# Kernel optimization log

Measured on AMD Instinct MI355X. Metric: run time of the kernel, lower is better.

Reference implementation:

```python
import jax, jax.numpy as jnp
import numpy as np

N_GROUPS = 1024   # n
L = 128           # keys per group
R = 4             # queries per group (nq[i] == R)
NQ_TOTAL = N_GROUPS * R
D_Q = 256
D_K = 256
D_Z = 256
D_V = 256


def setup_inputs() -> dict:
    key = jax.random.key(0)
    ks = jax.random.split(key, 8)
    nq = jnp.full((N_GROUPS,), R, dtype=jnp.int32)
    q = jax.random.normal(ks[0], (NQ_TOTAL, D_Q), dtype=jnp.float32)
    k = jax.random.normal(ks[1], (N_GROUPS, L, D_K), dtype=jnp.float32)
    v = jax.random.normal(ks[2], (N_GROUPS, L, D_V), dtype=jnp.float32)
    m = jax.random.uniform(ks[3], (N_GROUPS, L)) < 0.9
    m = m.at[:, 0].set(True)  # guarantee each row has at least one valid key
    Wq = jax.random.normal(ks[4], (D_Q, D_Z), dtype=jnp.float32) / np.sqrt(D_Q)
    bq = jnp.zeros((D_Z,), dtype=jnp.float32)
    Wk = jax.random.normal(ks[5], (D_K, D_Z), dtype=jnp.float32) / np.sqrt(D_K)
    bk = jnp.zeros((D_Z,), dtype=jnp.float32)
    return {"nq": nq, "q": q, "k": k, "v": v, "m": m,
            "Wq": Wq, "bq": bq, "Wk": Wk, "bk": bk}


def reference(nq, q, v, k, m, Wq, bq, Wk, bk):
    # Linear projections (nn.Linear with bias)
    qz = q @ Wq + bq                      # (N, d_z)
    kz = k @ Wk + bk                      # (n, l, d_z)
    d_z = Wq.shape[1]
    n = m.shape[0]
    # group index per query: equivalent to repeat_interleave(nq, 0)
    gidx = jnp.repeat(jnp.arange(n), nq, total_repeat_length=q.shape[0])  # (N,)
    # scores: s[i, l] = <kz[group(i), l], qz[i]> / sqrt(d_z)
    s = jnp.einsum('ild,id->il', kz[gidx], qz) / jnp.sqrt(jnp.asarray(d_z, qz.dtype))
    s = jnp.where(m[gidx], s, -jnp.inf)   # masked_fill(~m, -inf)
    p = jax.nn.softmax(s, axis=-1)        # softmax over key dim l
    # weighted sum over keys: (N, d)
    return jnp.einsum('il,ild->id', p, v[gidx])
```

## Files before the change

### kernel.cpp

```cpp
#include <hip/hip_runtime.h>

#define D 256
#define LKEYS 128
#define NGROUP 1024
#define NQ 4096

#define MMAT_OFF 0
#define RVEC_OFF (D * D)
#define U_OFF    (RVEC_OFF + D)
#define WS_FLOATS (U_OFF + NQ * D)

#define DOT4(a, b) ((a).x*(b).x + (a).y*(b).y + (a).z*(b).z + (a).w*(b).w)

__device__ __forceinline__ void gload_lds16(const float* g, float* l) {
    __builtin_amdgcn_global_load_lds(
        (const __attribute__((address_space(1))) void*)g,
        (__attribute__((address_space(3))) void*)l, 16, 0, 0);
}

__global__ __launch_bounds__(256) void prep_kernel(
    const float* __restrict__ Wq, const float* __restrict__ Wk,
    const float* __restrict__ bq, float* __restrict__ Mmat,
    float* __restrict__ rvec)
{
    __shared__ float wq_s[32][65];
    __shared__ float wk_s[32][65];
    __shared__ float bq_s[64];
    const int t  = threadIdx.x;
    const int a0 = (int)(blockIdx.x >> 3) * 32;
    const int b0 = (int)(blockIdx.x & 7) * 32;
    const int ai = t >> 4;
    const int bj = t & 15;
    float acc00 = 0.f, acc01 = 0.f, acc10 = 0.f, acc11 = 0.f;
    float racc = 0.f;
    for (int z0 = 0; z0 < D; z0 += 64) {
        __syncthreads();
        #pragma unroll
        for (int i = 0; i < 2; ++i) {
            const int f4i = t + 256 * i;
            const int row = f4i >> 4;
            const int c   = (f4i & 15) * 4;
            float4 aa = *(const float4*)&Wq[(size_t)(a0 + row) * D + z0 + c];
            wq_s[row][c] = aa.x; wq_s[row][c+1] = aa.y; wq_s[row][c+2] = aa.z; wq_s[row][c+3] = aa.w;
            float4 bb = *(const float4*)&Wk[(size_t)(b0 + row) * D + z0 + c];
            wk_s[row][c] = bb.x; wk_s[row][c+1] = bb.y; wk_s[row][c+2] = bb.z; wk_s[row][c+3] = bb.w;
        }
        if (t < 64) bq_s[t] = bq[z0 + t];
        __syncthreads();
        #pragma unroll 8
        for (int z = 0; z < 64; ++z) {
            const float wq0 = wq_s[ai][z];
            const float wq1 = wq_s[ai + 16][z];
            const float wk0 = wk_s[bj][z];
            const float wk1 = wk_s[bj + 16][z];
            acc00 += wq0 * wk0; acc01 += wq0 * wk1;
            acc10 += wq1 * wk0; acc11 += wq1 * wk1;
        }
        if (a0 == 0 && t < 32) {
            #pragma unroll 8
            for (int z = 0; z < 64; ++z) racc += bq_s[z] * wk_s[t][z];
        }
    }
    Mmat[(size_t)(a0 + ai)      * D + b0 + bj]      = acc00;
    Mmat[(size_t)(a0 + ai)      * D + b0 + bj + 16] = acc01;
    Mmat[(size_t)(a0 + ai + 16) * D + b0 + bj]      = acc10;
    Mmat[(size_t)(a0 + ai + 16) * D + b0 + bj + 16] = acc11;
    if (a0 == 0 && t < 32) rvec[b0 + t] = racc;
}

__global__ __launch_bounds__(256) void u_gemm_kernel(
    const float* __restrict__ q, const float* __restrict__ Mmat,
    const float* __restrict__ rvec, float* __restrict__ uout)
{
    __shared__ float q_s[16][D];
    const int b = blockIdx.x, t = threadIdx.x, lane = t & 63, w = t >> 6;
    {
        const float4* qg = (const float4*)(q + (size_t)b * 16 * D);
        float4* qs4 = (float4*)q_s;
        #pragma unroll
        for (int i = 0; i < 4; ++i) qs4[t + 256 * i] = qg[t + 256 * i];
    }
    __syncthreads();

    const float4* M4 = (const float4*)Mmat;
    const int r0 = w * 4;
    float4 a0 = {0,0,0,0}, a1 = {0,0,0,0}, a2 = {0,0,0,0}, a3 = {0,0,0,0};
    #pragma unroll 4
    for (int kk = 0; kk < D; ++kk) {
        const float4 m4 = M4[kk * 64 + lane];
        const float qa = q_s[r0 + 0][kk], qb = q_s[r0 + 1][kk];
        const float qc = q_s[r0 + 2][kk], qd = q_s[r0 + 3][kk];
        a0.x += qa*m4.x; a0.y += qa*m4.y; a0.z += qa*m4.z; a0.w += qa*m4.w;
        a1.x += qb*m4.x; a1.y += qb*m4.y; a1.z += qb*m4.z; a1.w += qb*m4.w;
        a2.x += qc*m4.x; a2.y += qc*m4.y; a2.z += qc*m4.z; a2.w += qc*m4.w;
        a3.x += qd*m4.x; a3.y += qd*m4.y; a3.z += qd*m4.z; a3.w += qd*m4.w;
    }
    const float4 r4 = ((const float4*)rvec)[lane];
    float4* U4 = (float4*)uout;
    float4 o;
    o.x=(a0.x+r4.x)*0.0625f; o.y=(a0.y+r4.y)*0.0625f; o.z=(a0.z+r4.z)*0.0625f; o.w=(a0.w+r4.w)*0.0625f;
    U4[((size_t)b * 16 + r0 + 0) * 64 + lane] = o;
    o.x=(a1.x+r4.x)*0.0625f; o.y=(a1.y+r4.y)*0.0625f; o.z=(a1.z+r4.z)*0.0625f; o.w=(a1.w+r4.w)*0.0625f;
    U4[((size_t)b * 16 + r0 + 1) * 64 + lane] = o;
    o.x=(a2.x+r4.x)*0.0625f; o.y=(a2.y+r4.y)*0.0625f; o.z=(a2.z+r4.z)*0.0625f; o.w=(a2.w+r4.w)*0.0625f;
    U4[((size_t)b * 16 + r0 + 2) * 64 + lane] = o;
    o.x=(a3.x+r4.x)*0.0625f; o.y=(a3.y+r4.y)*0.0625f; o.z=(a3.z+r4.z)*0.0625f; o.w=(a3.w+r4.w)*0.0625f;
    U4[((size_t)b * 16 + r0 + 3) * 64 + lane] = o;
}

__global__ __launch_bounds__(256) void attn2_kernel(
    const float* __restrict__ k, const float* __restrict__ v,
    const int* __restrict__ m, const float* __restrict__ uws,
    float* __restrict__ out)
{
    const int g = blockIdx.x, t = threadIdx.x, lane = t & 63, w = t >> 6;

    __shared__ float buf[2][16 * D];
    __shared__ float p_s[4][LKEYS];
    __shared__ int   m_s[LKEYS];

    const float* kg = k + (size_t)g * LKEYS * D;
    const float* vg = v + (size_t)g * LKEYS * D;

    auto stage = [&](const float* src, int tile, int b) {
        const float* s = src + (size_t)tile * 16 * D;
        #pragma unroll
        for (int j = 0; j < 4; ++j) {
            const int r = w * 4 + j;
            gload_lds16(s + r * D + lane * 4, &buf[b][r * D]);
        }
    };

    stage(kg, 0, 0);
    if (t < LKEYS) m_s[t] = m[(size_t)g * LKEYS + t];

    const float4* U4 = (const float4*)uws;
    const float4 u0 = U4[((size_t)g * 4 + 0) * 64 + lane];
    const float4 u1 = U4[((size_t)g * 4 + 1) * 64 + lane];
    const float4 u2 = U4[((size_t)g * 4 + 2) * 64 + lane];
    const float4 u3 = U4[((size_t)g * 4 + 3) * 64 + lane];
    __syncthreads();

    for (int tl = 0; tl < 8; ++tl) {
        if (tl < 7) stage(kg, tl + 1, (tl + 1) & 1);

        const float4* B4 = (const float4*)&buf[tl & 1][0];
        const int kb = w * 4;
        const float4 ka0 = B4[(kb + 0) * 64 + lane];
        const float4 ka1 = B4[(kb + 1) * 64 + lane];
        const float4 ka2 = B4[(kb + 2) * 64 + lane];
        const float4 ka3 = B4[(kb + 3) * 64 + lane];

        float v16[16];
        v16[ 0]=DOT4(ka0,u0); v16[ 1]=DOT4(ka0,u1); v16[ 2]=DOT4(ka0,u2); v16[ 3]=DOT4(ka0,u3);
        v16[ 4]=DOT4(ka1,u0); v16[ 5]=DOT4(ka1,u1); v16[ 6]=DOT4(ka1,u2); v16[ 7]=DOT4(ka1,u3);
        v16[ 8]=DOT4(ka2,u0); v16[ 9]=DOT4(ka2,u1); v16[10]=DOT4(ka2,u2); v16[11]=DOT4(ka2,u3);
        v16[12]=DOT4(ka3,u0); v16[13]=DOT4(ka3,u1); v16[14]=DOT4(ka3,u2); v16[15]=DOT4(ka3,u3);

        float v8[8];
        { const int hb = lane & 1;
          #pragma unroll
          for (int i = 0; i < 8; ++i) {
              const float keep = hb ? v16[8 + i] : v16[i];
              const float send = hb ? v16[i]     : v16[8 + i];
              v8[i] = keep + __shfl_xor(send, 1);
          } }
        float v4a[4];
        { const int hb = (lane >> 1) & 1;
          #pragma unroll
          for (int i = 0; i < 4; ++i) {
              const float keep = hb ? v8[4 + i] : v8[i];
              const float send = hb ? v8[i]     : v8[4 + i];
              v4a[i] = keep + __shfl_xor(send, 2);
          } }
        float v2a[2];
        { const int hb = (lane >> 2) & 1;
          #pragma unroll
          for (int i = 0; i < 2; ++i) {
              const float keep = hb ? v4a[2 + i] : v4a[i];
              const float send = hb ? v4a[i]     : v4a[2 + i];
              v2a[i] = keep + __shfl_xor(send, 4);
          } }
        float v1;
        { const int hb = (lane >> 3) & 1;
          const float keep = hb ? v2a[1] : v2a[0];
          const float send = hb ? v2a[0] : v2a[1];
          v1 = keep + __shfl_xor(send, 8); }
        v1 += __shfl_xor(v1, 16);
        v1 += __shfl_xor(v1, 32);

        if (lane < 16) {
            const int i  = ((lane & 1) << 3) | ((lane & 2) << 1) | ((lane & 4) >> 1) | ((lane & 8) >> 3);
            const int kl = tl * 16 + w * 4 + (i >> 2);
            p_s[i & 3][kl] = m_s[kl] ? v1 : -1e30f;
        }
        __syncthreads();
    }

    stage(vg, 0, 0);
    {
        const float s0 = p_s[w][lane];
        const float s1 = p_s[w][lane + 64];
        float mx = fmaxf(s0, s1);
        #pragma unroll
        for (int off = 32; off > 0; off >>= 1) mx = fmaxf(mx, __shfl_xor(mx, off));
        const float e0 = __expf(s0 - mx);
        const float e1 = __expf(s1 - mx);
        float sm = e0 + e1;
        #pragma unroll
        for (int off = 32; off > 0; off >>= 1) sm += __shfl_xor(sm, off);
        const float inv = 1.0f / sm;
        p_s[w][lane]      = e0 * inv;
        p_s[w][lane + 64] = e1 * inv;
    }
    __syncthreads();

    float4 acc = {0, 0, 0, 0};
    for (int tl = 0; tl < 8; ++tl) {
        if (tl < 7) stage(vg, tl + 1, (tl + 1) & 1);
        const float4* B4 = (const float4*)&buf[tl & 1][0];
        #pragma unroll
        for (int r = 0; r < 16; ++r) {
            const float pw = p_s[w][tl * 16 + r];
            const float4 vv = B4[r * 64 + lane];
            acc.x += pw * vv.x; acc.y += pw * vv.y;
            acc.z += pw * vv.z; acc.w += pw * vv.w;
        }
        __syncthreads();
    }
    ((float4*)(out + ((size_t)g * 4 + w) * D))[lane] = acc;
}

__global__ __launch_bounds__(256) void attn_kernel(
    const float* __restrict__ q, const float* __restrict__ k,
    const float* __restrict__ v, const int* __restrict__ m,
    const float* __restrict__ Mmat, const float* __restrict__ rvec,
    float* __restrict__ out)
{
    const int g    = blockIdx.x;
    const int t    = threadIdx.x;
    const int lane = t & 63;
    const int w    = t >> 6;

    __shared__ float  q_s[4][D];
    __shared__ float4 part_s[4][4][64];
    __shared__ float4 u_s4[4][64];
    __shared__ float  p_s[4][LKEYS];
    __shared__ int    m_s[LKEYS];

    {
        const float4* qg = (const float4*)(q + (size_t)g * 4 * D);
        ((float4*)q_s)[t] = qg[t];
    }
    if (t < LKEYS) m_s[t] = m[(size_t)g * LKEYS + t];
    __syncthreads();
    {
        const float4* M4 = (const float4*)Mmat;
        float4 p0 = {0,0,0,0}, p1 = {0,0,0,0}, p2 = {0,0,0,0}, p3 = {0,0,0,0};
        const int base = w * 64;
        #pragma unroll 4
        for (int dd = 0; dd < 64; ++dd) {
            const int a = base + dd;
            const float4 m4 = M4[a * 64 + lane];
            const float q0 = q_s[0][a], q1 = q_s[1][a], q2 = q_s[2][a], q3 = q_s[3][a];
            p0.x += q0*m4.x; p0.y += q0*m4.y; p0.z += q0*m4.z; p0.w += q0*m4.w;
            p1.x += q1*m4.x; p1.y += q1*m4.y; p1.z += q1*m4.z; p1.w += q1*m4.w;
            p2.x += q2*m4.x; p2.y += q2*m4.y; p2.z += q2*m4.z; p2.w += q2*m4.w;
            p3.x += q3*m4.x; p3.y += q3*m4.y; p3.z += q3*m4.z; p3.w += q3*m4.w;
        }
        part_s[w][0][lane] = p0; part_s[w][1][lane] = p1;
        part_s[w][2][lane] = p2; part_s[w][3][lane] = p3;
    }
    __syncthreads();
    {
        float4 acc = ((const float4*)rvec)[lane];
        const float4 a0 = part_s[0][w][lane], a1 = part_s[1][w][lane];
        const float4 a2 = part_s[2][w][lane], a3 = part_s[3][w][lane];
        acc.x += a0.x + a1.x + a2.x + a3.x;
        acc.y += a0.y + a1.y + a2.y + a3.y;
        acc.z += a0.z + a1.z + a2.z + a3.z;
        acc.w += a0.w + a1.w + a2.w + a3.w;
        u_s4[w][lane] = acc;
    }
    __syncthreads();

    const float4 u0 = u_s4[0][lane], u1 = u_s4[1][lane];
    const float4 u2 = u_s4[2][lane], u3 = u_s4[3][lane];
    {
        const float4* kg = (const float4*)(k + (size_t)g * LKEYS * D);
        auto reduce_qt = [&](float d0, float d1, float d2, float d3) -> float {
            float keepA = (lane & 1) ? d1 : d0;
            float sendA = (lane & 1) ? d0 : d1;
            keepA += __shfl_xor(sendA, 1);
            float keepB = (lane & 1) ? d3 : d2;
            float sendB = (lane & 1) ? d2 : d3;
            keepB += __shfl_xor(sendB, 1);
            float keep = (lane & 2) ? keepB : keepA;
            float send = (lane & 2) ? keepA : keepB;
            keep += __shfl_xor(send, 2);
            keep += __shfl_xor(keep, 4);
            keep += __shfl_xor(keep, 8);
            keep += __shfl_xor(keep, 16);
            keep += __shfl_xor(keep, 32);
            return keep;
        };
        const int l0 = w * 32;
        for (int kk = 0; kk < 32; kk += 4) {
            const int l = l0 + kk;
            const float4 kA = kg[(l + 0) * 64 + lane];
            const float4 kB = kg[(l + 1) * 64 + lane];
            const float4 kC = kg[(l + 2) * 64 + lane];
            const float4 kD = kg[(l + 3) * 64 + lane];
            float dA0 = DOT4(kA,u0), dA1 = DOT4(kA,u1), dA2 = DOT4(kA,u2), dA3 = DOT4(kA,u3);
            float dB0 = DOT4(kB,u0), dB1 = DOT4(kB,u1), dB2 = DOT4(kB,u2), dB3 = DOT4(kB,u3);
            float dC0 = DOT4(kC,u0), dC1 = DOT4(kC,u1), dC2 = DOT4(kC,u2), dC3 = DOT4(kC,u3);
            float dD0 = DOT4(kD,u0), dD1 = DOT4(kD,u1), dD2 = DOT4(kD,u2), dD3 = DOT4(kD,u3);
            const float rA = reduce_qt(dA0, dA1, dA2, dA3);
            const float rB = reduce_qt(dB0, dB1, dB2, dB3);
            const float rC = reduce_qt(dC0, dC1, dC2, dC3);
            const float rD = reduce_qt(dD0, dD1, dD2, dD3);
            if (lane < 4) {
                p_s[lane][l + 0] = m_s[l + 0] ? rA * 0.0625f : -1e30f;
                p_s[lane][l + 1] = m_s[l + 1] ? rB * 0.0625f : -1e30f;
                p_s[lane][l + 2] = m_s[l + 2] ? rC * 0.0625f : -1e30f;
                p_s[lane][l + 3] = m_s[l + 3] ? rD * 0.0625f : -1e30f;
            }
        }
    }
    __syncthreads();
    {
        const float v0 = p_s[w][lane];
        const float v1 = p_s[w][lane + 64];
        float mx = fmaxf(v0, v1);
        #pragma unroll
        for (int off = 32; off > 0; off >>= 1) mx = fmaxf(mx, __shfl_xor(mx, off));
        const float e0 = __expf(v0 - mx);
        const float e1 = __expf(v1 - mx);
        float sm = e0 + e1;
        #pragma unroll
        for (int off = 32; off > 0; off >>= 1) sm += __shfl_xor(sm, off);
        const float inv = 1.0f / sm;
        p_s[w][lane]      = e0 * inv;
        p_s[w][lane + 64] = e1 * inv;
    }
    {
        const float4* vg = (const float4*)(v + (size_t)g * LKEYS * D);
        float4 acc = {0,0,0,0};
        #pragma unroll 8
        for (int l = 0; l < LKEYS; ++l) {
            const float pw = p_s[w][l];
            const float4 vv = vg[l * 64 + lane];
            acc.x += pw * vv.x; acc.y += pw * vv.y;
            acc.z += pw * vv.z; acc.w += pw * vv.w;
        }
        float4* og = (float4*)(out + ((size_t)g * 4 + w) * D);
        og[lane] = acc;
    }
}

extern "C" void kernel_launch(void* const* d_in, const int* in_sizes, int n_in,
                              void* d_out, int out_size, void* d_ws, size_t ws_size,
                              hipStream_t stream) {
    const float* q  = (const float*)d_in[1];
    const float* k  = (const float*)d_in[2];
    const float* v  = (const float*)d_in[3];
    const int*   m  = (const int*)  d_in[4];
    const float* Wq = (const float*)d_in[5];
    const float* bq = (const float*)d_in[6];
    const float* Wk = (const float*)d_in[7];

    float* ws = (float*)d_ws;
    prep_kernel<<<64, 256, 0, stream>>>(Wq, Wk, bq, ws + MMAT_OFF, ws + RVEC_OFF);

    if (ws_size >= (size_t)WS_FLOATS * sizeof(float)) {
        u_gemm_kernel<<<NQ / 16, 256, 0, stream>>>(q, ws + MMAT_OFF, ws + RVEC_OFF, ws + U_OFF);
        attn2_kernel<<<NGROUP, 256, 0, stream>>>(k, v, m, ws + U_OFF, (float*)d_out);
    } else {
        attn_kernel<<<NGROUP, 256, 0, stream>>>(q, k, v, m, ws + MMAT_OFF, ws + RVEC_OFF,
                                                (float*)d_out);
    }
}
```

Before: 81.14 us.

## Give each wave a private key slice and ring buffer to drop block barriers

The attention kernel is restructured so each wave owns 32 keys and a private 8-row LDS ring, streaming K then V through it with explicit vmcnt waits instead of block-wide __syncthreads per tile. The mask becomes a wave ballot, the softmax normalisation is deferred to the end, and partial P·V sums from the four waves are reduced through LDS. This is meant to remove per-tile barrier stalls and overlap V prefetch with the score phase. The cost is an extra cross-wave reduction and reliance on hand-placed waitcnt ordering, which is fragile.

```diff
diff --git a/kernel.cpp b/kernel.cpp
--- a/kernel.cpp
+++ b/kernel.cpp
@@ -17,6 +17,11 @@
         (const __attribute__((address_space(1))) void*)g,
         (__attribute__((address_space(3))) void*)l, 16, 0, 0);
 }
+
+#define WAITVM(N) do { asm volatile("s_waitcnt vmcnt(" #N ")" ::: "memory"); \
+                       __builtin_amdgcn_sched_barrier(0); } while (0)
+#define WAITLG0   do { asm volatile("s_waitcnt lgkmcnt(0)" ::: "memory"); \
+                       __builtin_amdgcn_sched_barrier(0); } while (0)
 
 __global__ __launch_bounds__(256) void prep_kernel(
     const float* __restrict__ Wq, const float* __restrict__ Wk,
@@ -108,54 +113,65 @@
     U4[((size_t)b * 16 + r0 + 3) * 64 + lane] = o;
 }
 
-__global__ __launch_bounds__(256) void attn2_kernel(
+__global__ __launch_bounds__(256, 4) void attn3_kernel(
     const float* __restrict__ k, const float* __restrict__ v,
     const int* __restrict__ m, const float* __restrict__ uws,
     float* __restrict__ out)
 {
     const int g = blockIdx.x, t = threadIdx.x, lane = t & 63, w = t >> 6;
 
-    __shared__ float buf[2][16 * D];
-    __shared__ float p_s[4][LKEYS];
-    __shared__ int   m_s[LKEYS];
-
-    const float* kg = k + (size_t)g * LKEYS * D;
-    const float* vg = v + (size_t)g * LKEYS * D;
-
-    auto stage = [&](const float* src, int tile, int b) {
-        const float* s = src + (size_t)tile * 16 * D;
-        #pragma unroll
-        for (int j = 0; j < 4; ++j) {
-            const int r = w * 4 + j;
-            gload_lds16(s + r * D + lane * 4, &buf[b][r * D]);
-        }
+    __shared__ float smem[4 * 8 * D + LKEYS * 4];
+    float* const myring = smem + w * 8 * D;
+    float* const p_t    = smem + 4 * 8 * D;
+
+    const int mk = (lane < 32) ? m[(size_t)g * LKEYS + w * 32 + lane] : 0;
+    const unsigned long long bal = __ballot(mk != 0);
+
+    const float4* U4 = (const float4*)(uws + (size_t)g * 4 * D);
+    const float4 u0 = U4[0 * 64 + lane];
+    const float4 u1 = U4[1 * 64 + lane];
+    const float4 u2 = U4[2 * 64 + lane];
+    const float4 u3 = U4[3 * 64 + lane];
+    asm volatile("s_waitcnt vmcnt(0)" ::: "memory");
+    __builtin_amdgcn_sched_barrier(0);
+
+    const float* kg = k + ((size_t)g * LKEYS + w * 32) * D;
+    const float* vg = v + ((size_t)g * LKEYS + w * 32) * D;
+
+    auto issueK = [&](int c) {
+        const int sl = (4 * c) & 7;
+        #pragma unroll
+        for (int j = 0; j < 4; ++j)
+            gload_lds16(kg + (size_t)(4 * c + j) * D + lane * 4, myring + (sl + j) * D);
     };
-
-    stage(kg, 0, 0);
-    if (t < LKEYS) m_s[t] = m[(size_t)g * LKEYS + t];
-
-    const float4* U4 = (const float4*)uws;
-    const float4 u0 = U4[((size_t)g * 4 + 0) * 64 + lane];
-    const float4 u1 = U4[((size_t)g * 4 + 1) * 64 + lane];
-    const float4 u2 = U4[((size_t)g * 4 + 2) * 64 + lane];
-    const float4 u3 = U4[((size_t)g * 4 + 3) * 64 + lane];
-    __syncthreads();
-
-    for (int tl = 0; tl < 8; ++tl) {
-        if (tl < 7) stage(kg, tl + 1, (tl + 1) & 1);
-
-        const float4* B4 = (const float4*)&buf[tl & 1][0];
-        const int kb = w * 4;
-        const float4 ka0 = B4[(kb + 0) * 64 + lane];
-        const float4 ka1 = B4[(kb + 1) * 64 + lane];
-        const float4 ka2 = B4[(kb + 2) * 64 + lane];
-        const float4 ka3 = B4[(kb + 3) * 64 + lane];
+    auto issueV = [&](int c) {
+        const int sl = (4 * c) & 7;
+        #pragma unroll
+        for (int j = 0; j < 4; ++j)
+            gload_lds16(vg + (size_t)(4 * c + j) * D + lane * 4, myring + (sl + j) * D);
+    };
+
+    issueK(0); issueK(1);
+
+    #pragma unroll
+    for (int c = 0; c < 8; ++c) {
+        WAITVM(4);
+        const int sl = (4 * c) & 7;
+        const float4* R = (const float4*)myring;
+        const float4 k0 = R[(sl + 0) * 64 + lane];
+        const float4 k1 = R[(sl + 1) * 64 + lane];
+        const float4 k2 = R[(sl + 2) * 64 + lane];
+        const float4 k3 = R[(sl + 3) * 64 + lane];
+        WAITLG0;
+        if (c < 6)       issueK(c + 2);
+        else if (c == 6) issueV(0);
+        else             issueV(1);
 
         float v16[16];
-        v16[ 0]=DOT4(ka0,u0); v16[ 1]=DOT4(ka0,u1); v16[ 2]=DOT4(ka0,u2); v16[ 3]=DOT4(ka0,u3);
-        v16[ 4]=DOT4(ka1,u0); v16[ 5]=DOT4(ka1,u1); v16[ 6]=DOT4(ka1,u2); v16[ 7]=DOT4(ka1,u3);
-        v16[ 8]=DOT4(ka2,u0); v16[ 9]=DOT4(ka2,u1); v16[10]=DOT4(ka2,u2); v16[11]=DOT4(ka2,u3);
-        v16[12]=DOT4(ka3,u0); v16[13]=DOT4(ka3,u1); v16[14]=DOT4(ka3,u2); v16[15]=DOT4(ka3,u3);
+        v16[ 0]=DOT4(k0,u0); v16[ 1]=DOT4(k0,u1); v16[ 2]=DOT4(k0,u2); v16[ 3]=DOT4(k0,u3);
+        v16[ 4]=DOT4(k1,u0); v16[ 5]=DOT4(k1,u1); v16[ 6]=DOT4(k1,u2); v16[ 7]=DOT4(k1,u3);
+        v16[ 8]=DOT4(k2,u0); v16[ 9]=DOT4(k2,u1); v16[10]=DOT4(k2,u2); v16[11]=DOT4(k2,u3);
+        v16[12]=DOT4(k3,u0); v16[13]=DOT4(k3,u1); v16[14]=DOT4(k3,u2); v16[15]=DOT4(k3,u3);
 
         float v8[8];
         { const int hb = lane & 1;
@@ -191,44 +207,89 @@
 
         if (lane < 16) {
             const int i  = ((lane & 1) << 3) | ((lane & 2) << 1) | ((lane & 4) >> 1) | ((lane & 8) >> 3);
-            const int kl = tl * 16 + w * 4 + (i >> 2);
-            p_s[i & 3][kl] = m_s[kl] ? v1 : -1e30f;
-        }
-        __syncthreads();
-    }
-
-    stage(vg, 0, 0);
-    {
-        const float s0 = p_s[w][lane];
-        const float s1 = p_s[w][lane + 64];
+            const int kl = 4 * c + (i >> 2);
+            p_t[(w * 32 + kl) * 4 + (i & 3)] = ((bal >> kl) & 1ull) ? v1 : -1e30f;
+        }
+    }
+
+    WAITLG0;
+    __builtin_amdgcn_s_barrier();
+
+    float inv;
+    {
+        const float s0 = p_t[lane * 4 + w];
+        const float s1 = p_t[(lane + 64) * 4 + w];
         float mx = fmaxf(s0, s1);
         #pragma unroll
         for (int off = 32; off > 0; off >>= 1) mx = fmaxf(mx, __shfl_xor(mx, off));
         const float e0 = __expf(s0 - mx);
         const float e1 = __expf(s1 - mx);
-        float sm = e0 + e1;
-        #pragma unroll
-        for (int off = 32; off > 0; off >>= 1) sm += __shfl_xor(sm, off);
-        const float inv = 1.0f / sm;
-        p_s[w][lane]      = e0 * inv;
-        p_s[w][lane + 64] = e1 * inv;
-    }
-    __syncthreads();
-
-    float4 acc = {0, 0, 0, 0};
-    for (int tl = 0; tl < 8; ++tl) {
-        if (tl < 7) stage(vg, tl + 1, (tl + 1) & 1);
-        const float4* B4 = (const float4*)&buf[tl & 1][0];
-        #pragma unroll
-        for (int r = 0; r < 16; ++r) {
-            const float pw = p_s[w][tl * 16 + r];
-            const float4 vv = B4[r * 64 + lane];
-            acc.x += pw * vv.x; acc.y += pw * vv.y;
-            acc.z += pw * vv.z; acc.w += pw * vv.w;
-        }
-        __syncthreads();
-    }
-    ((float4*)(out + ((size_t)g * 4 + w) * D))[lane] = acc;
+        float su = e0 + e1;
+        #pragma unroll
+        for (int off = 32; off > 0; off >>= 1) su += __shfl_xor(su, off);
+        inv = 1.0f / su;
+        p_t[lane * 4 + w]        = e0;
+        p_t[(lane + 64) * 4 + w] = e1;
+    }
+    WAITLG0;
+    __builtin_amdgcn_s_barrier();
+
+    float4 a0 = {0,0,0,0}, a1 = {0,0,0,0}, a2 = {0,0,0,0}, a3 = {0,0,0,0};
+    #pragma unroll
+    for (int c = 0; c < 8; ++c) {
+        if (c < 7) { WAITVM(4); } else { WAITVM(0); }
+        const int sl = (4 * c) & 7;
+        const float4* R = (const float4*)myring;
+        const float4 w0 = R[(sl + 0) * 64 + lane];
+        const float4 w1 = R[(sl + 1) * 64 + lane];
+        const float4 w2 = R[(sl + 2) * 64 + lane];
+        const float4 w3 = R[(sl + 3) * 64 + lane];
+        const float4 p0 = *(const float4*)&p_t[(w * 32 + 4 * c + 0) * 4];
+        const float4 p1 = *(const float4*)&p_t[(w * 32 + 4 * c + 1) * 4];
+        const float4 p2 = *(const float4*)&p_t[(w * 32 + 4 * c + 2) * 4];
+        const float4 p3 = *(const float4*)&p_t[(w * 32 + 4 * c + 3) * 4];
+        WAITLG0;
+        if (c < 6) issueV(c + 2);
+
+        a0.x += p0.x*w0.x; a0.y += p0.x*w0.y; a0.z += p0.x*w0.z; a0.w += p0.x*w0.w;
+        a1.x += p0.y*w0.x; a1.y += p0.y*w0.y; a1.z += p0.y*w0.z; a1.w += p0.y*w0.w;
+        a2.x += p0.z*w0.x; a2.y += p0.z*w0.y; a2.z += p0.z*w0.z; a2.w += p0.z*w0.w;
+        a3.x += p0.w*w0.x; a3.y += p0.w*w0.y; a3.z += p0.w*w0.z; a3.w += p0.w*w0.w;
+        a0.x += p1.x*w1.x; a0.y += p1.x*w1.y; a0.z += p1.x*w1.z; a0.w += p1.x*w1.w;
+        a1.x += p1.y*w1.x; a1.y += p1.y*w1.y; a1.z += p1.y*w1.z; a1.w += p1.y*w1.w;
+        a2.x += p1.z*w1.x; a2.y += p1.z*w1.y; a2.z += p1.z*w1.z; a2.w += p1.z*w1.w;
+        a3.x += p1.w*w1.x; a3.y += p1.w*w1.y; a3.z += p1.w*w1.z; a3.w += p1.w*w1.w;
+        a0.x += p2.x*w2.x; a0.y += p2.x*w2.y; a0.z += p2.x*w2.z; a0.w += p2.x*w2.w;
+        a1.x += p2.y*w2.x; a1.y += p2.y*w2.y; a1.z += p2.y*w2.z; a1.w += p2.y*w2.w;
+        a2.x += p2.z*w2.x; a2.y += p2.z*w2.y; a2.z += p2.z*w2.z; a2.w += p2.z*w2.w;
+        a3.x += p2.w*w2.x; a3.y += p2.w*w2.y; a3.z += p2.w*w2.z; a3.w += p2.w*w2.w;
+        a0.x += p3.x*w3.x; a0.y += p3.x*w3.y; a0.z += p3.x*w3.z; a0.w += p3.x*w3.w;
+        a1.x += p3.y*w3.x; a1.y += p3.y*w3.y; a1.z += p3.y*w3.z; a1.w += p3.y*w3.w;
+        a2.x += p3.z*w3.x; a2.y += p3.z*w3.y; a2.z += p3.z*w3.z; a2.w += p3.z*w3.w;
+        a3.x += p3.w*w3.x; a3.y += p3.w*w3.y; a3.z += p3.w*w3.z; a3.w += p3.w*w3.w;
+    }
+
+    WAITLG0;
+    __builtin_amdgcn_s_barrier();
+    float4* part = (float4*)smem;
+    part[(w * 4 + 0) * 64 + lane] = a0;
+    part[(w * 4 + 1) * 64 + lane] = a1;
+    part[(w * 4 + 2) * 64 + lane] = a2;
+    part[(w * 4 + 3) * 64 + lane] = a3;
+    WAITLG0;
+    __builtin_amdgcn_s_barrier();
+    {
+        const float4 r0 = part[(0 * 4 + w) * 64 + lane];
+        const float4 r1 = part[(1 * 4 + w) * 64 + lane];
+        const float4 r2 = part[(2 * 4 + w) * 64 + lane];
+        const float4 r3 = part[(3 * 4 + w) * 64 + lane];
+        float4 o;
+        o.x = (r0.x + r1.x + r2.x + r3.x) * inv;
+        o.y = (r0.y + r1.y + r2.y + r3.y) * inv;
+        o.z = (r0.z + r1.z + r2.z + r3.z) * inv;
+        o.w = (r0.w + r1.w + r2.w + r3.w) * inv;
+        ((float4*)(out + ((size_t)g * 4 + w) * D))[lane] = o;
+    }
 }
 
 __global__ __launch_bounds__(256) void attn_kernel(
@@ -374,7 +435,7 @@
 
     if (ws_size >= (size_t)WS_FLOATS * sizeof(float)) {
         u_gemm_kernel<<<NQ / 16, 256, 0, stream>>>(q, ws + MMAT_OFF, ws + RVEC_OFF, ws + U_OFF);
-        attn2_kernel<<<NGROUP, 256, 0, stream>>>(k, v, m, ws + U_OFF, (float*)d_out);
+        attn3_kernel<<<NGROUP, 256, 0, stream>>>(k, v, m, ws + U_OFF, (float*)d_out);
     } else {
         attn_kernel<<<NGROUP, 256, 0, stream>>>(q, k, v, m, ws + MMAT_OFF, ws + RVEC_OFF,
                                                 (float*)d_out);
```

Result: slower. 97.37 us (+20.0%).

## Split keys across waves with direct global loads and cross-wave output reduction

Applied to the files above, without the earlier changes.

The attention kernel stops staging K/V tiles through LDS with async global-to-LDS copies and per-tile barriers. Each wave now owns a contiguous 32-key slice, reads K and V straight from global memory into registers, gets mask bits through a ballot, and computes partial outputs for all four queries. The partials are then summed across waves through shared memory. This removes most barriers and the large LDS buffer, which allows more resident blocks and more loads in flight. The cost is higher register use and an extra reduction step.

```diff
diff --git a/kernel.cpp b/kernel.cpp
--- a/kernel.cpp
+++ b/kernel.cpp
@@ -11,12 +11,6 @@
 #define WS_FLOATS (U_OFF + NQ * D)
 
 #define DOT4(a, b) ((a).x*(b).x + (a).y*(b).y + (a).z*(b).z + (a).w*(b).w)
-
-__device__ __forceinline__ void gload_lds16(const float* g, float* l) {
-    __builtin_amdgcn_global_load_lds(
-        (const __attribute__((address_space(1))) void*)g,
-        (__attribute__((address_space(3))) void*)l, 16, 0, 0);
-}
 
 __global__ __launch_bounds__(256) void prep_kernel(
     const float* __restrict__ Wq, const float* __restrict__ Wk,
@@ -108,48 +102,35 @@
     U4[((size_t)b * 16 + r0 + 3) * 64 + lane] = o;
 }
 
-__global__ __launch_bounds__(256) void attn2_kernel(
+__global__ __launch_bounds__(256, 4) void attn4_kernel(
     const float* __restrict__ k, const float* __restrict__ v,
     const int* __restrict__ m, const float* __restrict__ uws,
     float* __restrict__ out)
 {
     const int g = blockIdx.x, t = threadIdx.x, lane = t & 63, w = t >> 6;
 
-    __shared__ float buf[2][16 * D];
-    __shared__ float p_s[4][LKEYS];
-    __shared__ int   m_s[LKEYS];
-
-    const float* kg = k + (size_t)g * LKEYS * D;
-    const float* vg = v + (size_t)g * LKEYS * D;
-
-    auto stage = [&](const float* src, int tile, int b) {
-        const float* s = src + (size_t)tile * 16 * D;
-        #pragma unroll
-        for (int j = 0; j < 4; ++j) {
-            const int r = w * 4 + j;
-            gload_lds16(s + r * D + lane * 4, &buf[b][r * D]);
-        }
-    };
-
-    stage(kg, 0, 0);
-    if (t < LKEYS) m_s[t] = m[(size_t)g * LKEYS + t];
-
-    const float4* U4 = (const float4*)uws;
-    const float4 u0 = U4[((size_t)g * 4 + 0) * 64 + lane];
-    const float4 u1 = U4[((size_t)g * 4 + 1) * 64 + lane];
-    const float4 u2 = U4[((size_t)g * 4 + 2) * 64 + lane];
-    const float4 u3 = U4[((size_t)g * 4 + 3) * 64 + lane];
-    __syncthreads();
-
-    for (int tl = 0; tl < 8; ++tl) {
-        if (tl < 7) stage(kg, tl + 1, (tl + 1) & 1);
-
-        const float4* B4 = (const float4*)&buf[tl & 1][0];
-        const int kb = w * 4;
-        const float4 ka0 = B4[(kb + 0) * 64 + lane];
-        const float4 ka1 = B4[(kb + 1) * 64 + lane];
-        const float4 ka2 = B4[(kb + 2) * 64 + lane];
-        const float4 ka3 = B4[(kb + 3) * 64 + lane];
+    __shared__ float4 part_s[4][4][64];
+    __shared__ float  p_t[LKEYS][4];
+
+    const float4* U4 = (const float4*)(uws + (size_t)g * 4 * D);
+    const float4 u0 = U4[0 * 64 + lane];
+    const float4 u1 = U4[1 * 64 + lane];
+    const float4 u2 = U4[2 * 64 + lane];
+    const float4 u3 = U4[3 * 64 + lane];
+
+    const int mk = (lane < 32) ? m[(size_t)g * LKEYS + w * 32 + lane] : 0;
+    const unsigned long long bal = __ballot(mk != 0);
+
+    const float4* kg = (const float4*)(k + ((size_t)g * LKEYS + w * 32) * D);
+    const float4* vg = (const float4*)(v + ((size_t)g * LKEYS + w * 32) * D);
+
+    #pragma unroll
+    for (int it = 0; it < 8; ++it) {
+        const int kb = it * 4;
+        const float4 ka0 = kg[(kb + 0) * 64 + lane];
+        const float4 ka1 = kg[(kb + 1) * 64 + lane];
+        const float4 ka2 = kg[(kb + 2) * 64 + lane];
+        const float4 ka3 = kg[(kb + 3) * 64 + lane];
 
         float v16[16];
         v16[ 0]=DOT4(ka0,u0); v16[ 1]=DOT4(ka0,u1); v16[ 2]=DOT4(ka0,u2); v16[ 3]=DOT4(ka0,u3);
@@ -191,44 +172,62 @@
 
         if (lane < 16) {
             const int i  = ((lane & 1) << 3) | ((lane & 2) << 1) | ((lane & 4) >> 1) | ((lane & 8) >> 3);
-            const int kl = tl * 16 + w * 4 + (i >> 2);
-            p_s[i & 3][kl] = m_s[kl] ? v1 : -1e30f;
-        }
-        __syncthreads();
-    }
-
-    stage(vg, 0, 0);
-    {
-        const float s0 = p_s[w][lane];
-        const float s1 = p_s[w][lane + 64];
+            const int kl = kb + (i >> 2);
+            p_t[w * 32 + kl][i & 3] = ((bal >> kl) & 1ull) ? v1 : -1e30f;
+        }
+    }
+    __syncthreads();
+
+    {
+        const float s0 = p_t[lane][w];
+        const float s1 = p_t[lane + 64][w];
         float mx = fmaxf(s0, s1);
         #pragma unroll
         for (int off = 32; off > 0; off >>= 1) mx = fmaxf(mx, __shfl_xor(mx, off));
         const float e0 = __expf(s0 - mx);
         const float e1 = __expf(s1 - mx);
-        float sm = e0 + e1;
-        #pragma unroll
-        for (int off = 32; off > 0; off >>= 1) sm += __shfl_xor(sm, off);
-        const float inv = 1.0f / sm;
-        p_s[w][lane]      = e0 * inv;
-        p_s[w][lane + 64] = e1 * inv;
-    }
-    __syncthreads();
-
-    float4 acc = {0, 0, 0, 0};
-    for (int tl = 0; tl < 8; ++tl) {
-        if (tl < 7) stage(vg, tl + 1, (tl + 1) & 1);
-        const float4* B4 = (const float4*)&buf[tl & 1][0];
-        #pragma unroll
-        for (int r = 0; r < 16; ++r) {
-            const float pw = p_s[w][tl * 16 + r];
-            const float4 vv = B4[r * 64 + lane];
-            acc.x += pw * vv.x; acc.y += pw * vv.y;
-            acc.z += pw * vv.z; acc.w += pw * vv.w;
-        }
-        __syncthreads();
-    }
-    ((float4*)(out + ((size_t)g * 4 + w) * D))[lane] = acc;
+        float su = e0 + e1;
+        #pragma unroll
+        for (int off = 32; off > 0; off >>= 1) su += __shfl_xor(su, off);
+        const float inv = 1.0f / su;
+        p_t[lane][w]      = e0 * inv;
+        p_t[lane + 64][w] = e1 * inv;
+    }
+    __syncthreads();
+
+    float4 a0 = {0,0,0,0}, a1 = {0,0,0,0}, a2 = {0,0,0,0}, a3 = {0,0,0,0};
+    #pragma unroll
+    for (int it = 0; it < 4; ++it) {
+        const int base = it * 8;
+        float4 va[8];
+        #pragma unroll
+        for (int j = 0; j < 8; ++j) va[j] = vg[(base + j) * 64 + lane];
+        #pragma unroll
+        for (int j = 0; j < 8; ++j) {
+            const float4 pr = *(const float4*)&p_t[w * 32 + base + j][0];
+            const float4 vv = va[j];
+            a0.x += pr.x*vv.x; a0.y += pr.x*vv.y; a0.z += pr.x*vv.z; a0.w += pr.x*vv.w;
+            a1.x += pr.y*vv.x; a1.y += pr.y*vv.y; a1.z += pr.y*vv.z; a1.w += pr.y*vv.w;
+            a2.x += pr.z*vv.x; a2.y += pr.z*vv.y; a2.z += pr.z*vv.z; a2.w += pr.z*vv.w;
+            a3.x += pr.w*vv.x; a3.y += pr.w*vv.y; a3.z += pr.w*vv.z; a3.w += pr.w*vv.w;
+        }
+    }
+
+    part_s[w][0][lane] = a0; part_s[w][1][lane] = a1;
+    part_s[w][2][lane] = a2; part_s[w][3][lane] = a3;
+    __syncthreads();
+    {
+        const float4 r0 = part_s[0][w][lane];
+        const float4 r1 = part_s[1][w][lane];
+        const float4 r2 = part_s[2][w][lane];
+        const float4 r3 = part_s[3][w][lane];
+        float4 o;
+        o.x = r0.x + r1.x + r2.x + r3.x;
+        o.y = r0.y + r1.y + r2.y + r3.y;
+        o.z = r0.z + r1.z + r2.z + r3.z;
+        o.w = r0.w + r1.w + r2.w + r3.w;
+        ((float4*)(out + ((size_t)g * 4 + w) * D))[lane] = o;
+    }
 }
 
 __global__ __launch_bounds__(256) void attn_kernel(
@@ -374,7 +373,7 @@
 
     if (ws_size >= (size_t)WS_FLOATS * sizeof(float)) {
         u_gemm_kernel<<<NQ / 16, 256, 0, stream>>>(q, ws + MMAT_OFF, ws + RVEC_OFF, ws + U_OFF);
-        attn2_kernel<<<NGROUP, 256, 0, stream>>>(k, v, m, ws + U_OFF, (float*)d_out);
+        attn4_kernel<<<NGROUP, 256, 0, stream>>>(k, v, m, ws + U_OFF, (float*)d_out);
     } else {
         attn_kernel<<<NGROUP, 256, 0, stream>>>(q, k, v, m, ws + MMAT_OFF, ws + RVEC_OFF,
                                                 (float*)d_out);
```

Measured after the change: 83.70 us. 3.2% more time.
